# Optimization experiments

Hardware: AMD Instinct MI355X
Metric: run time of the kernel (lower is better)

## Reference

```python
import jax, jax.numpy as jnp
import numpy as np

B, NX, NY = 4, 16384, 16384
CX = CY = 256
CK = CV = 256
H = 8


def setup_inputs() -> dict:
    key = jax.random.key(0)
    ks = jax.random.split(key, 12)
    s = 0.02
    return {
        "x": jax.random.normal(ks[0], (B, NX, CX), jnp.float32),
        "y": jax.random.normal(ks[1], (B, NY, CY), jnp.float32),
        "x_pos_embed": jax.random.normal(ks[2], (B, NX, CX), jnp.float32),
        "y_pos_embed": jax.random.normal(ks[3], (B, NY, CY), jnp.float32),
        "Wq": jax.random.normal(ks[4], (CK, CX), jnp.float32) * s,
        "bq": jnp.zeros((CK,), jnp.float32),
        "Wk": jax.random.normal(ks[5], (CK, CY), jnp.float32) * s,
        "bk": jnp.zeros((CK,), jnp.float32),
        "Wv": jax.random.normal(ks[6], (CV, CY), jnp.float32) * s,
        "bv": jnp.zeros((CV,), jnp.float32),
        "Wr": jax.random.normal(ks[7], (CX, CV), jnp.float32) * s,
        "br": jnp.zeros((CX,), jnp.float32),
    }


def reference(x, y, x_pos_embed, y_pos_embed, Wq, bq, Wk, bk, Wv, bv, Wr, br):
    # Linear projections (nn.Linear: x @ W.T + b)
    q = (x + x_pos_embed) @ Wq.T + bq            # [B, Nx, Ck]
    k = (y + y_pos_embed) @ Wk.T + bk            # [B, Ny, Ck]
    v = y @ Wv.T + bv                            # [B, Ny, Cv]

    dk, dv = CK // H, CV // H
    # Split heads: [B, N, H, d] -> [B, H, N, d]
    q = q.reshape(B, NX, H, dk).transpose(0, 2, 1, 3)
    k = k.reshape(B, NY, H, dk).transpose(0, 2, 1, 3)
    v = v.reshape(B, NY, H, dv).transpose(0, 2, 1, 3)

    # key softmax over tokens (Ny); query softmax over per-head channels (dk)
    k = jax.nn.softmax(k, axis=2)                # [B, H, Ny, dk]
    q = jax.nn.softmax(q, axis=3)                # [B, H, Nx, dk]

    # context = softmax(K)^T V : [B, H, dk, dv]
    context = jnp.einsum('bhnk,bhnv->bhkv', k, v)
    # attended = Q context : [B, H, Nx, dv]
    attended = jnp.einsum('bhnk,bhkv->bhnv', q, context)

    # merge heads -> [B, Nx, Cv], reproject -> [B, Nx, Cx]
    agg = attended.transpose(0, 2, 1, 3).reshape(B, NX, CV)
    return agg @ Wr.T + br
```

## Files before the change

### kernel.cpp

```cpp
#include <hip/hip_runtime.h>


typedef float f32x4 __attribute__((ext_vector_type(4)));
typedef short s16x4 __attribute__((ext_vector_type(4)));
typedef short s16x8 __attribute__((ext_vector_type(8)));

#define MFMA16(A, B, C) __builtin_amdgcn_mfma_f32_16x16x32_bf16((A), (B), (C), 0, 0, 0)

__device__ __forceinline__ short f2bf(float f) {
    unsigned u = __builtin_bit_cast(unsigned, f);
    u = (u + 0x7FFFu + ((u >> 16) & 1u)) >> 16;
    return (short)u;
}
__device__ __forceinline__ float bf2f(short b) {
    unsigned u = ((unsigned)(unsigned short)b) << 16;
    return __builtin_bit_cast(float, u);
}

__global__ __launch_bounds__(256) void wcvt_kernel(
    const float* __restrict__ wq, const float* __restrict__ wk,
    const float* __restrict__ wv, const float* __restrict__ wr,
    short* __restrict__ wbf)
{
    int id = blockIdx.x * 256 + threadIdx.x;
    int m = id >> 13;
    int slot = id & 8191;
    int tile = slot >> 9;
    int ks   = (slot >> 6) & 7;
    int lane = slot & 63;
    int lrow = lane & 15, lgrp = lane >> 4;
    const float* src = (m == 0) ? wq : (m == 1) ? wk : (m == 2) ? wv : wr;
    const float* p = src + (size_t)(tile * 16 + lrow) * 256 + ks * 32 + lgrp * 8;
    f32x4 a = *(const f32x4*)p;
    f32x4 b = *(const f32x4*)(p + 4);
    s16x8 o;
    o[0]=f2bf(a[0]); o[1]=f2bf(a[1]); o[2]=f2bf(a[2]); o[3]=f2bf(a[3]);
    o[4]=f2bf(b[0]); o[5]=f2bf(b[1]); o[6]=f2bf(b[2]); o[7]=f2bf(b[3]);
    *(s16x8*)(wbf + (size_t)id * 8) = o;
}

__global__ __launch_bounds__(256, 4) void kv_kernel(
    const float* __restrict__ y, const float* __restrict__ ypos,
    const short* __restrict__ wkp, const short* __restrict__ wvp,
    const float* __restrict__ bk, const float* __restrict__ bv,
    short* __restrict__ e_buf, short* __restrict__ v_buf)
{
    __shared__ short smem[32 * 512];
    short* ak = smem;
    short* av = smem + 32 * 256;
    const int row0 = blockIdx.x * 32;
    const int t = threadIdx.x;
    const int w = t >> 6, lane = t & 63;

    {
        #pragma unroll
        for (int it = 0; it < 8; ++it) {
            int r = it * 4 + w;
            const float* sy = y    + (size_t)(row0 + r) * 256 + lane * 4;
            const float* sp = ypos + (size_t)(row0 + r) * 256 + lane * 4;
            f32x4 a = *(const f32x4*)sy;
            f32x4 p = *(const f32x4*)sp;
            f32x4 k = a + p;
            s16x4 ov, ok;
            ov[0]=f2bf(a[0]); ov[1]=f2bf(a[1]); ov[2]=f2bf(a[2]); ov[3]=f2bf(a[3]);
            ok[0]=f2bf(k[0]); ok[1]=f2bf(k[1]); ok[2]=f2bf(k[2]); ok[3]=f2bf(k[3]);
            int swz = ((lane >> 1) ^ (r & 7)) * 8 + (lane & 1) * 4;
            *(s16x4*)(av + r * 256 + swz) = ov;
            *(s16x4*)(ak + r * 256 + swz) = ok;
        }
    }
    __syncthreads();

    const int lrow = lane & 15, lgrp = lane >> 4;
    const bool is_k = (w < 2);
    const int colbase = (w & 1) * 128;
    const short* WP = is_k ? wkp : wvp;
    const float* bp = is_k ? bk : bv;
    const short* A = is_k ? ak : av;

    float bias[8];
    #pragma unroll
    for (int nf = 0; nf < 8; ++nf) bias[nf] = bp[colbase + nf * 16 + lrow];

    s16x8 af[2][8];
    #pragma unroll
    for (int mf = 0; mf < 2; ++mf) {
        int rr = mf * 16 + lrow;
        #pragma unroll
        for (int ks = 0; ks < 8; ++ks) {
            int cs = ((ks * 4 + lgrp) ^ (rr & 7));
            af[mf][ks] = *(const s16x8*)(A + rr * 256 + cs * 8);
        }
    }
    __syncthreads();

    #pragma unroll
    for (int nf = 0; nf < 8; ++nf) {
        const int tile = (colbase >> 4) + nf;
        const short* wt = WP + ((size_t)tile * 8) * 512 + lane * 8;
        f32x4 a0 = (f32x4){0.f, 0.f, 0.f, 0.f};
        f32x4 a1 = (f32x4){0.f, 0.f, 0.f, 0.f};
        #pragma unroll
        for (int kg = 0; kg < 2; ++kg) {
            s16x8 bf[4];
            #pragma unroll
            for (int kk = 0; kk < 4; ++kk)
                bf[kk] = *(const s16x8*)(wt + (kg * 4 + kk) * 512);
            #pragma unroll
            for (int kk = 0; kk < 4; ++kk) {
                a0 = MFMA16(af[0][kg * 4 + kk], bf[kk], a0);
                a1 = MFMA16(af[1][kg * 4 + kk], bf[kk], a1);
            }
        }
        const int colp = (is_k ? 0 : 256) + colbase + nf * 16 + lrow;
        #pragma unroll
        for (int rr = 0; rr < 4; ++rr) {
            float v0 = a0[rr] + bias[nf];
            float v1 = a1[rr] + bias[nf];
            if (is_k) { v0 = __expf(v0); v1 = __expf(v1); }
            int lr0 = lgrp * 4 + rr;
            int lr1 = lr0 + 16;
            smem[lr0 * 512 + (((colp >> 3) ^ (lr0 & 7)) * 8) + (colp & 7)] = f2bf(v0);
            smem[lr1 * 512 + (((colp >> 3) ^ (lr1 & 7)) * 8) + (colp & 7)] = f2bf(v1);
        }
    }
    __syncthreads();

    {
        #pragma unroll
        for (int i = 0; i < 8; ++i) {
            int r = i * 4 + w;
            int grow = row0 + r;
            s16x8 val = *(const s16x8*)(smem + r * 512 + (lane ^ (r & 7)) * 8);
            if (lane < 32)
                *(s16x8*)(e_buf + (size_t)grow * 256 + lane * 8) = val;
            else
                *(s16x8*)(v_buf + (size_t)grow * 256 + (lane - 32) * 8) = val;
        }
    }
}

__global__ __launch_bounds__(256) void ctx_kernel(
    const short* __restrict__ e_buf, const short* __restrict__ v_buf,
    float* __restrict__ partials)
{
    __shared__ float se[128 * 32];
    __shared__ float sv[128 * 32];
    __shared__ float red[4 * 1056];
    const int cb = blockIdx.x, bh = blockIdx.y;
    const int b = bh >> 3, h = bh & 7;
    const int tok0 = b * 16384 + cb * 1024;
    const int t = threadIdx.x, w = t >> 6, lane = t & 63;
    const int ckb = (lane >> 3) * 4, cvb = (lane & 7) * 4;

    f32x4 acc[4];
    #pragma unroll
    for (int i = 0; i < 4; ++i) acc[i] = (f32x4){0.f, 0.f, 0.f, 0.f};
    f32x4 dn = (f32x4){0.f, 0.f, 0.f, 0.f};

    for (int it = 0; it < 8; ++it) {
        __syncthreads();
        #pragma unroll
        for (int s = 0; s < 2; ++s) {
            int id = t + s * 256;
            int rr = id >> 2, pp = id & 3;
            size_t g = (size_t)(tok0 + it * 128 + rr) * 256 + h * 32 + pp * 8;
            s16x8 ee = *(const s16x8*)(e_buf + g);
            s16x8 vv = *(const s16x8*)(v_buf + g);
            f32x4 e0 = {bf2f(ee[0]), bf2f(ee[1]), bf2f(ee[2]), bf2f(ee[3])};
            f32x4 e1 = {bf2f(ee[4]), bf2f(ee[5]), bf2f(ee[6]), bf2f(ee[7])};
            f32x4 v0 = {bf2f(vv[0]), bf2f(vv[1]), bf2f(vv[2]), bf2f(vv[3])};
            f32x4 v1 = {bf2f(vv[4]), bf2f(vv[5]), bf2f(vv[6]), bf2f(vv[7])};
            *(f32x4*)(se + rr * 32 + pp * 8)     = e0;
            *(f32x4*)(se + rr * 32 + pp * 8 + 4) = e1;
            *(f32x4*)(sv + rr * 32 + pp * 8)     = v0;
            *(f32x4*)(sv + rr * 32 + pp * 8 + 4) = v1;
        }
        __syncthreads();
        const int r0 = w * 32;
        #pragma unroll 8
        for (int rr = 0; rr < 32; ++rr) {
            f32x4 e4 = *(const f32x4*)(se + (r0 + rr) * 32 + ckb);
            f32x4 v4 = *(const f32x4*)(sv + (r0 + rr) * 32 + cvb);
            acc[0] += e4[0] * v4;
            acc[1] += e4[1] * v4;
            acc[2] += e4[2] * v4;
            acc[3] += e4[3] * v4;
            dn += e4;
        }
    }
    __syncthreads();
    #pragma unroll
    for (int i = 0; i < 4; ++i)
        *(f32x4*)(red + w * 1056 + (ckb + i) * 32 + cvb) = acc[i];
    if ((lane & 7) == 0)
        *(f32x4*)(red + w * 1056 + 1024 + ckb) = dn;
    __syncthreads();
    float* outp = partials + (size_t)(bh * 16 + cb) * 1056;
    for (int e = t; e < 1056; e += 256)
        outp[e] = red[e] + red[1056 + e] + red[2112 + e] + red[3168 + e];
}

__global__ __launch_bounds__(256) void ctx_reduce_kernel(
    const float* __restrict__ partials, short* __restrict__ ctxT)
{
    __shared__ float s[1056];
    const int bh = blockIdx.x, t = threadIdx.x;
    for (int e = t; e < 1056; e += 256) {
        float a = 0.f;
        for (int c = 0; c < 16; ++c) a += partials[(size_t)(bh * 16 + c) * 1056 + e];
        s[e] = a;
    }
    __syncthreads();
    for (int e = t; e < 1024; e += 256) {
        int ck = e >> 5, cv = e & 31;
        float val = s[e] / s[1024 + ck];
        ctxT[(size_t)bh * 1024 + cv * 32 + ck] = f2bf(val);
    }
}

__global__ __launch_bounds__(256, 4) void qout_kernel(
    const float* __restrict__ x, const float* __restrict__ xpos,
    const short* __restrict__ wqp, const float* __restrict__ bq,
    const short* __restrict__ ctxT,
    const short* __restrict__ wrp, const float* __restrict__ br,
    float* __restrict__ out)
{
    __shared__ short alds[32 * 256];
    __shared__ short qlds[4][32 * 64];
    const int row0 = blockIdx.x * 32;
    const int b = row0 >> 14;
    const int t = threadIdx.x;
    const int w = t >> 6, lane = t & 63;

    {
        #pragma unroll
        for (int it = 0; it < 8; ++it) {
            int r = it * 4 + w;
            const float* sx = x    + (size_t)(row0 + r) * 256 + lane * 4;
            const float* sp = xpos + (size_t)(row0 + r) * 256 + lane * 4;
            f32x4 a = *(const f32x4*)sx;
            f32x4 p = *(const f32x4*)sp;
            a += p;
            s16x4 o;
            o[0]=f2bf(a[0]); o[1]=f2bf(a[1]); o[2]=f2bf(a[2]); o[3]=f2bf(a[3]);
            int swz = ((lane >> 1) ^ (r & 7)) * 8 + (lane & 1) * 4;
            *(s16x4*)(alds + r * 256 + swz) = o;
        }
    }
    __syncthreads();

    const int lrow = lane & 15, lgrp = lane >> 4;
    const int wc = w * 64;

    float biasq[4];
    #pragma unroll
    for (int nf = 0; nf < 4; ++nf) biasq[nf] = bq[wc + nf * 16 + lrow];

    f32x4 acc[2][4];
    #pragma unroll
    for (int mf = 0; mf < 2; ++mf)
        #pragma unroll
        for (int nf = 0; nf < 4; ++nf) acc[mf][nf] = (f32x4){0.f, 0.f, 0.f, 0.f};

    #pragma unroll
    for (int ks = 0; ks < 8; ++ks) {
        s16x8 af[2];
        #pragma unroll
        for (int mf = 0; mf < 2; ++mf) {
            int rr = mf * 16 + lrow;
            int cs = (ks * 4 + lgrp) ^ (rr & 7);
            af[mf] = *(const s16x8*)(alds + rr * 256 + cs * 8);
        }
        #pragma unroll
        for (int nf = 0; nf < 4; ++nf) {
            int tile = (wc >> 4) + nf;
            s16x8 bfr = *(const s16x8*)(wqp + ((size_t)tile * 8 + ks) * 512 + lane * 8);
            acc[0][nf] = MFMA16(af[0], bfr, acc[0][nf]);
            acc[1][nf] = MFMA16(af[1], bfr, acc[1][nf]);
        }
    }

    short* ql = (short*)qlds[w];
    #pragma unroll
    for (int mf = 0; mf < 2; ++mf) {
        f32x4 e[4];
        #pragma unroll
        for (int nf = 0; nf < 4; ++nf)
            #pragma unroll
            for (int rr = 0; rr < 4; ++rr)
                e[nf][rr] = __expf(acc[mf][nf][rr] + biasq[nf]);
        #pragma unroll
        for (int hl = 0; hl < 2; ++hl) {
            #pragma unroll
            for (int rr = 0; rr < 4; ++rr) {
                float s = e[hl * 2][rr] + e[hl * 2 + 1][rr];
                s += __shfl_xor(s, 1);
                s += __shfl_xor(s, 2);
                s += __shfl_xor(s, 4);
                s += __shfl_xor(s, 8);
                float rinv = 1.0f / s;
                int row = mf * 16 + lgrp * 4 + rr;
                #pragma unroll
                for (int n2 = 0; n2 < 2; ++n2) {
                    int colc = hl * 32 + n2 * 16 + lrow;
                    int cs = (colc >> 3) ^ (row & 7);
                    ql[row * 64 + cs * 8 + (colc & 7)] = f2bf(e[hl * 2 + n2][rr] * rinv);
                }
            }
        }
    }
    __syncthreads();

    f32x4 att[2][2][2];
    #pragma unroll
    for (int hl = 0; hl < 2; ++hl)
        #pragma unroll
        for (int mf = 0; mf < 2; ++mf)
            #pragma unroll
            for (int n2 = 0; n2 < 2; ++n2) att[hl][mf][n2] = (f32x4){0.f,0.f,0.f,0.f};

    #pragma unroll
    for (int hl = 0; hl < 2; ++hl) {
        const short* cbase = ctxT + (size_t)(b * 8 + w * 2 + hl) * 1024;
        s16x8 bctx[2];
        #pragma unroll
        for (int n2 = 0; n2 < 2; ++n2)
            bctx[n2] = *(const s16x8*)(cbase + (n2 * 16 + lrow) * 32 + lgrp * 8);
        #pragma unroll
        for (int mf = 0; mf < 2; ++mf) {
            int row = mf * 16 + lrow;
            int cs = (hl * 4 + lgrp) ^ (row & 7);
            s16x8 aq = *(const s16x8*)(ql + row * 64 + cs * 8);
            #pragma unroll
            for (int n2 = 0; n2 < 2; ++n2)
                att[hl][mf][n2] = MFMA16(aq, bctx[n2], att[hl][mf][n2]);
        }
    }

    #pragma unroll
    for (int hl = 0; hl < 2; ++hl)
      #pragma unroll
      for (int mf = 0; mf < 2; ++mf)
        #pragma unroll
        for (int n2 = 0; n2 < 2; ++n2)
          #pragma unroll
          for (int rr = 0; rr < 4; ++rr) {
              int row = mf * 16 + lgrp * 4 + rr;
              int col = wc + hl * 32 + n2 * 16 + lrow;
              int cs = (col >> 3) ^ (row & 7);
              alds[row * 256 + cs * 8 + (col & 7)] = f2bf(att[hl][mf][n2][rr]);
          }
    __syncthreads();

    float biasr[4];
    #pragma unroll
    for (int nf = 0; nf < 4; ++nf) biasr[nf] = br[wc + nf * 16 + lrow];

    f32x4 acc2[2][4];
    #pragma unroll
    for (int mf = 0; mf < 2; ++mf)
        #pragma unroll
        for (int nf = 0; nf < 4; ++nf) acc2[mf][nf] = (f32x4){0.f, 0.f, 0.f, 0.f};

    #pragma unroll
    for (int ks = 0; ks < 8; ++ks) {
        s16x8 af[2];
        #pragma unroll
        for (int mf = 0; mf < 2; ++mf) {
            int rr = mf * 16 + lrow;
            int cs = (ks * 4 + lgrp) ^ (rr & 7);
            af[mf] = *(const s16x8*)(alds + rr * 256 + cs * 8);
        }
        #pragma unroll
        for (int nf = 0; nf < 4; ++nf) {
            int tile = (wc >> 4) + nf;
            s16x8 bfr = *(const s16x8*)(wrp + ((size_t)tile * 8 + ks) * 512 + lane * 8);
            acc2[0][nf] = MFMA16(af[0], bfr, acc2[0][nf]);
            acc2[1][nf] = MFMA16(af[1], bfr, acc2[1][nf]);
        }
    }

    #pragma unroll
    for (int mf = 0; mf < 2; ++mf)
      #pragma unroll
      for (int nf = 0; nf < 4; ++nf)
        #pragma unroll
        for (int rr = 0; rr < 4; ++rr) {
            int grow = row0 + mf * 16 + lgrp * 4 + rr;
            out[(size_t)grow * 256 + wc + nf * 16 + lrow] = acc2[mf][nf][rr] + biasr[nf];
        }
}

extern "C" void kernel_launch(void* const* d_in, const int* in_sizes, int n_in,
                              void* d_out, int out_size, void* d_ws, size_t ws_size,
                              hipStream_t stream)
{
    const float* x    = (const float*)d_in[0];
    const float* y    = (const float*)d_in[1];
    const float* xpos = (const float*)d_in[2];
    const float* ypos = (const float*)d_in[3];
    const float* Wq   = (const float*)d_in[4];
    const float* bq   = (const float*)d_in[5];
    const float* Wk   = (const float*)d_in[6];
    const float* bk   = (const float*)d_in[7];
    const float* Wv   = (const float*)d_in[8];
    const float* bv   = (const float*)d_in[9];
    const float* Wr   = (const float*)d_in[10];
    const float* br   = (const float*)d_in[11];

    char*  ws    = (char*)d_ws;
    short* wbf   = (short*)(ws);
    short* ctxT  = (short*)(ws + 524288);
    float* parts = (float*)(ws + (1 << 20));
    short* e_buf = (short*)(ws + ((size_t)4 << 20));
    short* v_buf = e_buf + (size_t)65536 * 256;
    float* outp  = (float*)d_out;

    hipLaunchKernelGGL(wcvt_kernel, dim3(128), dim3(256), 0, stream,
                       Wq, Wk, Wv, Wr, wbf);
    hipLaunchKernelGGL(kv_kernel, dim3(2048), dim3(256), 0, stream,
                       y, ypos, wbf + 65536, wbf + 131072, bk, bv, e_buf, v_buf);
    hipLaunchKernelGGL(ctx_kernel, dim3(16, 32), dim3(256), 0, stream,
                       e_buf, v_buf, parts);
    hipLaunchKernelGGL(ctx_reduce_kernel, dim3(32), dim3(256), 0, stream,
                       parts, ctxT);
    hipLaunchKernelGGL(qout_kernel, dim3(2048), dim3(256), 0, stream,
                       x, xpos, wbf, bq, ctxT, wbf + 196608, br, outp);
}
```

Baseline: 169.1 us.

## Use 512-thread blocks in kv and qout kernels, one 16-row tile per wave

```diff
diff --git a/kernel.cpp b/kernel.cpp
--- a/kernel.cpp
+++ b/kernel.cpp
@@ -39,7 +39,7 @@
     *(s16x8*)(wbf + (size_t)id * 8) = o;
 }
 
-__global__ __launch_bounds__(256, 4) void kv_kernel(
+__global__ __launch_bounds__(512, 6) void kv_kernel(
     const float* __restrict__ y, const float* __restrict__ ypos,
     const short* __restrict__ wkp, const short* __restrict__ wvp,
     const float* __restrict__ bk, const float* __restrict__ bv,
@@ -54,12 +54,10 @@
 
     {
         #pragma unroll
-        for (int it = 0; it < 8; ++it) {
-            int r = it * 4 + w;
-            const float* sy = y    + (size_t)(row0 + r) * 256 + lane * 4;
-            const float* sp = ypos + (size_t)(row0 + r) * 256 + lane * 4;
-            f32x4 a = *(const f32x4*)sy;
-            f32x4 p = *(const f32x4*)sp;
+        for (int it = 0; it < 4; ++it) {
+            int r = it * 8 + w;
+            f32x4 a = *(const f32x4*)(y    + (size_t)(row0 + r) * 256 + lane * 4);
+            f32x4 p = *(const f32x4*)(ypos + (size_t)(row0 + r) * 256 + lane * 4);
             f32x4 k = a + p;
             s16x4 ov, ok;
             ov[0]=f2bf(a[0]); ov[1]=f2bf(a[1]); ov[2]=f2bf(a[2]); ov[3]=f2bf(a[3]);
@@ -72,8 +70,12 @@
     __syncthreads();
 
     const int lrow = lane & 15, lgrp = lane >> 4;
-    const bool is_k = (w < 2);
-    const int colbase = (w & 1) * 128;
+    const bool is_k = (w < 4);
+    const int sub = w & 3;
+    const int rh = sub >> 1;
+    const int ch = sub & 1;
+    const int colbase = ch * 128;
+    const int tile0 = ch * 8;
     const short* WP = is_k ? wkp : wvp;
     const float* bp = is_k ? bk : bv;
     const short* A = is_k ? ak : av;
@@ -82,56 +84,46 @@
     #pragma unroll
     for (int nf = 0; nf < 8; ++nf) bias[nf] = bp[colbase + nf * 16 + lrow];
 
-    s16x8 af[2][8];
-    #pragma unroll
-    for (int mf = 0; mf < 2; ++mf) {
-        int rr = mf * 16 + lrow;
+    s16x8 af[8];
+    {
+        int rr = rh * 16 + lrow;
         #pragma unroll
         for (int ks = 0; ks < 8; ++ks) {
             int cs = ((ks * 4 + lgrp) ^ (rr & 7));
-            af[mf][ks] = *(const s16x8*)(A + rr * 256 + cs * 8);
+            af[ks] = *(const s16x8*)(A + rr * 256 + cs * 8);
         }
     }
     __syncthreads();
 
     #pragma unroll
     for (int nf = 0; nf < 8; ++nf) {
-        const int tile = (colbase >> 4) + nf;
+        const int tile = tile0 + nf;
         const short* wt = WP + ((size_t)tile * 8) * 512 + lane * 8;
         f32x4 a0 = (f32x4){0.f, 0.f, 0.f, 0.f};
-        f32x4 a1 = (f32x4){0.f, 0.f, 0.f, 0.f};
-        #pragma unroll
-        for (int kg = 0; kg < 2; ++kg) {
-            s16x8 bf[4];
-            #pragma unroll
-            for (int kk = 0; kk < 4; ++kk)
-                bf[kk] = *(const s16x8*)(wt + (kg * 4 + kk) * 512);
-            #pragma unroll
-            for (int kk = 0; kk < 4; ++kk) {
-                a0 = MFMA16(af[0][kg * 4 + kk], bf[kk], a0);
-                a1 = MFMA16(af[1][kg * 4 + kk], bf[kk], a1);
-            }
+        #pragma unroll
+        for (int kg = 0; kg < 4; ++kg) {
+            s16x8 b0 = *(const s16x8*)(wt + (kg * 2 + 0) * 512);
+            s16x8 b1 = *(const s16x8*)(wt + (kg * 2 + 1) * 512);
+            a0 = MFMA16(af[kg * 2 + 0], b0, a0);
+            a0 = MFMA16(af[kg * 2 + 1], b1, a0);
         }
         const int colp = (is_k ? 0 : 256) + colbase + nf * 16 + lrow;
         #pragma unroll
         for (int rr = 0; rr < 4; ++rr) {
             float v0 = a0[rr] + bias[nf];
-            float v1 = a1[rr] + bias[nf];
-            if (is_k) { v0 = __expf(v0); v1 = __expf(v1); }
-            int lr0 = lgrp * 4 + rr;
-            int lr1 = lr0 + 16;
-            smem[lr0 * 512 + (((colp >> 3) ^ (lr0 & 7)) * 8) + (colp & 7)] = f2bf(v0);
-            smem[lr1 * 512 + (((colp >> 3) ^ (lr1 & 7)) * 8) + (colp & 7)] = f2bf(v1);
-        }
-    }
-    __syncthreads();
-
-    {
-        #pragma unroll
-        for (int i = 0; i < 8; ++i) {
-            int r = i * 4 + w;
+            if (is_k) v0 = __expf(v0);
+            int lr = rh * 16 + lgrp * 4 + rr;
+            smem[lr * 512 + (((colp >> 3) ^ (lr & 7)) * 8) + (colp & 7)] = f2bf(v0);
+        }
+    }
+    __syncthreads();
+
+    {
+        #pragma unroll
+        for (int i = 0; i < 4; ++i) {
+            int r = i * 8 + w;
             int grow = row0 + r;
-            s16x8 val = *(const s16x8*)(smem + r * 512 + (lane ^ (r & 7)) * 8);
+            s16x8 val = *(const s16x8*)(smem + r * 512 + ((lane ^ (r & 7)) << 3));
             if (lane < 32)
                 *(s16x8*)(e_buf + (size_t)grow * 256 + lane * 8) = val;
             else
@@ -219,7 +211,7 @@
     }
 }
 
-__global__ __launch_bounds__(256, 4) void qout_kernel(
+__global__ __launch_bounds__(512, 6) void qout_kernel(
     const float* __restrict__ x, const float* __restrict__ xpos,
     const short* __restrict__ wqp, const float* __restrict__ bq,
     const short* __restrict__ ctxT,
@@ -227,7 +219,7 @@
     float* __restrict__ out)
 {
     __shared__ short alds[32 * 256];
-    __shared__ short qlds[4][32 * 64];
+    __shared__ short qlds[8][16 * 64];
     const int row0 = blockIdx.x * 32;
     const int b = row0 >> 14;
     const int t = threadIdx.x;
@@ -235,12 +227,10 @@
 
     {
         #pragma unroll
-        for (int it = 0; it < 8; ++it) {
-            int r = it * 4 + w;
-            const float* sx = x    + (size_t)(row0 + r) * 256 + lane * 4;
-            const float* sp = xpos + (size_t)(row0 + r) * 256 + lane * 4;
-            f32x4 a = *(const f32x4*)sx;
-            f32x4 p = *(const f32x4*)sp;
+        for (int it = 0; it < 4; ++it) {
+            int r = it * 8 + w;
+            f32x4 a = *(const f32x4*)(x    + (size_t)(row0 + r) * 256 + lane * 4);
+            f32x4 p = *(const f32x4*)(xpos + (size_t)(row0 + r) * 256 + lane * 4);
             a += p;
             s16x4 o;
             o[0]=f2bf(a[0]); o[1]=f2bf(a[1]); o[2]=f2bf(a[2]); o[3]=f2bf(a[3]);
@@ -251,45 +241,49 @@
     __syncthreads();
 
     const int lrow = lane & 15, lgrp = lane >> 4;
-    const int wc = w * 64;
+    const int rh = w >> 2;
+    const int q4 = w & 3;
+    const int wc = q4 * 64;
+    const int tile0 = wc >> 4;
 
     float biasq[4];
     #pragma unroll
     for (int nf = 0; nf < 4; ++nf) biasq[nf] = bq[wc + nf * 16 + lrow];
 
-    f32x4 acc[2][4];
-    #pragma unroll
-    for (int mf = 0; mf < 2; ++mf)
-        #pragma unroll
-        for (int nf = 0; nf < 4; ++nf) acc[mf][nf] = (f32x4){0.f, 0.f, 0.f, 0.f};
-
-    #pragma unroll
-    for (int ks = 0; ks < 8; ++ks) {
-        s16x8 af[2];
-        #pragma unroll
-        for (int mf = 0; mf < 2; ++mf) {
-            int rr = mf * 16 + lrow;
+    s16x8 af[8];
+    {
+        int rr = rh * 16 + lrow;
+        #pragma unroll
+        for (int ks = 0; ks < 8; ++ks) {
             int cs = (ks * 4 + lgrp) ^ (rr & 7);
-            af[mf] = *(const s16x8*)(alds + rr * 256 + cs * 8);
-        }
-        #pragma unroll
-        for (int nf = 0; nf < 4; ++nf) {
-            int tile = (wc >> 4) + nf;
-            s16x8 bfr = *(const s16x8*)(wqp + ((size_t)tile * 8 + ks) * 512 + lane * 8);
-            acc[0][nf] = MFMA16(af[0], bfr, acc[0][nf]);
-            acc[1][nf] = MFMA16(af[1], bfr, acc[1][nf]);
+            af[ks] = *(const s16x8*)(alds + rr * 256 + cs * 8);
+        }
+    }
+
+    f32x4 acc[4];
+    #pragma unroll
+    for (int nf = 0; nf < 4; ++nf) acc[nf] = (f32x4){0.f, 0.f, 0.f, 0.f};
+
+    #pragma unroll
+    for (int nf = 0; nf < 4; ++nf) {
+        const short* wt = wqp + ((size_t)(tile0 + nf) * 8) * 512 + lane * 8;
+        #pragma unroll
+        for (int kg = 0; kg < 4; ++kg) {
+            s16x8 b0 = *(const s16x8*)(wt + (kg * 2 + 0) * 512);
+            s16x8 b1 = *(const s16x8*)(wt + (kg * 2 + 1) * 512);
+            acc[nf] = MFMA16(af[kg * 2 + 0], b0, acc[nf]);
+            acc[nf] = MFMA16(af[kg * 2 + 1], b1, acc[nf]);
         }
     }
 
     short* ql = (short*)qlds[w];
-    #pragma unroll
-    for (int mf = 0; mf < 2; ++mf) {
+    {
         f32x4 e[4];
         #pragma unroll
         for (int nf = 0; nf < 4; ++nf)
             #pragma unroll
             for (int rr = 0; rr < 4; ++rr)
-                e[nf][rr] = __expf(acc[mf][nf][rr] + biasq[nf]);
+                e[nf][rr] = __expf(acc[nf][rr] + biasq[nf]);
         #pragma unroll
         for (int hl = 0; hl < 2; ++hl) {
             #pragma unroll
@@ -300,95 +294,84 @@
                 s += __shfl_xor(s, 4);
                 s += __shfl_xor(s, 8);
                 float rinv = 1.0f / s;
-                int row = mf * 16 + lgrp * 4 + rr;
+                int lr = lgrp * 4 + rr;
                 #pragma unroll
                 for (int n2 = 0; n2 < 2; ++n2) {
                     int colc = hl * 32 + n2 * 16 + lrow;
-                    int cs = (colc >> 3) ^ (row & 7);
-                    ql[row * 64 + cs * 8 + (colc & 7)] = f2bf(e[hl * 2 + n2][rr] * rinv);
+                    int cs = (colc >> 3) ^ (lr & 7);
+                    ql[lr * 64 + cs * 8 + (colc & 7)] = f2bf(e[hl * 2 + n2][rr] * rinv);
                 }
             }
         }
     }
     __syncthreads();
 
-    f32x4 att[2][2][2];
+    f32x4 att[2][2];
     #pragma unroll
     for (int hl = 0; hl < 2; ++hl)
         #pragma unroll
-        for (int mf = 0; mf < 2; ++mf)
-            #pragma unroll
-            for (int n2 = 0; n2 < 2; ++n2) att[hl][mf][n2] = (f32x4){0.f,0.f,0.f,0.f};
+        for (int n2 = 0; n2 < 2; ++n2) att[hl][n2] = (f32x4){0.f,0.f,0.f,0.f};
 
     #pragma unroll
     for (int hl = 0; hl < 2; ++hl) {
-        const short* cbase = ctxT + (size_t)(b * 8 + w * 2 + hl) * 1024;
-        s16x8 bctx[2];
-        #pragma unroll
-        for (int n2 = 0; n2 < 2; ++n2)
-            bctx[n2] = *(const s16x8*)(cbase + (n2 * 16 + lrow) * 32 + lgrp * 8);
-        #pragma unroll
-        for (int mf = 0; mf < 2; ++mf) {
-            int row = mf * 16 + lrow;
-            int cs = (hl * 4 + lgrp) ^ (row & 7);
-            s16x8 aq = *(const s16x8*)(ql + row * 64 + cs * 8);
-            #pragma unroll
-            for (int n2 = 0; n2 < 2; ++n2)
-                att[hl][mf][n2] = MFMA16(aq, bctx[n2], att[hl][mf][n2]);
-        }
+        const short* cbase = ctxT + (size_t)(b * 8 + q4 * 2 + hl) * 1024;
+        s16x8 bctx0 = *(const s16x8*)(cbase + (0 * 16 + lrow) * 32 + lgrp * 8);
+        s16x8 bctx1 = *(const s16x8*)(cbase + (1 * 16 + lrow) * 32 + lgrp * 8);
+        int cs = (hl * 4 + lgrp) ^ (lrow & 7);
+        s16x8 aq = *(const s16x8*)(ql + lrow * 64 + cs * 8);
+        att[hl][0] = MFMA16(aq, bctx0, att[hl][0]);
+        att[hl][1] = MFMA16(aq, bctx1, att[hl][1]);
     }
 
     #pragma unroll
     for (int hl = 0; hl < 2; ++hl)
       #pragma unroll
-      for (int mf = 0; mf < 2; ++mf)
-        #pragma unroll
-        for (int n2 = 0; n2 < 2; ++n2)
-          #pragma unroll
-          for (int rr = 0; rr < 4; ++rr) {
-              int row = mf * 16 + lgrp * 4 + rr;
-              int col = wc + hl * 32 + n2 * 16 + lrow;
-              int cs = (col >> 3) ^ (row & 7);
-              alds[row * 256 + cs * 8 + (col & 7)] = f2bf(att[hl][mf][n2][rr]);
-          }
+      for (int n2 = 0; n2 < 2; ++n2)
+        #pragma unroll
+        for (int rr = 0; rr < 4; ++rr) {
+            int row = rh * 16 + lgrp * 4 + rr;
+            int col = wc + hl * 32 + n2 * 16 + lrow;
+            int cs = (col >> 3) ^ (row & 7);
+            alds[row * 256 + cs * 8 + (col & 7)] = f2bf(att[hl][n2][rr]);
+        }
     __syncthreads();
 
     float biasr[4];
     #pragma unroll
     for (int nf = 0; nf < 4; ++nf) biasr[nf] = br[wc + nf * 16 + lrow];
 
-    f32x4 acc2[2][4];
-    #pragma unroll
-    for (int mf = 0; mf < 2; ++mf)
-        #pragma unroll
-        for (int nf = 0; nf < 4; ++nf) acc2[mf][nf] = (f32x4){0.f, 0.f, 0.f, 0.f};
-
-    #pragma unroll
-    for (int ks = 0; ks < 8; ++ks) {
-        s16x8 af[2];
-        #pragma unroll
-        for (int mf = 0; mf < 2; ++mf) {
-            int rr = mf * 16 + lrow;
+    s16x8 af2[8];
+    {
+        int rr = rh * 16 + lrow;
+        #pragma unroll
+        for (int ks = 0; ks < 8; ++ks) {
             int cs = (ks * 4 + lgrp) ^ (rr & 7);
-            af[mf] = *(const s16x8*)(alds + rr * 256 + cs * 8);
-        }
-        #pragma unroll
-        for (int nf = 0; nf < 4; ++nf) {
-            int tile = (wc >> 4) + nf;
-            s16x8 bfr = *(const s16x8*)(wrp + ((size_t)tile * 8 + ks) * 512 + lane * 8);
-            acc2[0][nf] = MFMA16(af[0], bfr, acc2[0][nf]);
-            acc2[1][nf] = MFMA16(af[1], bfr, acc2[1][nf]);
-        }
-    }
-
-    #pragma unroll
-    for (int mf = 0; mf < 2; ++mf)
-      #pragma unroll
-      for (int nf = 0; nf < 4; ++nf)
+            af2[ks] = *(const s16x8*)(alds + rr * 256 + cs * 8);
+        }
+    }
+
+    f32x4 acc2[4];
+    #pragma unroll
+    for (int nf = 0; nf < 4; ++nf) acc2[nf] = (f32x4){0.f, 0.f, 0.f, 0.f};
+
+    #pragma unroll
+    for (int nf = 0; nf < 4; ++nf) {
+        const short* wt = wrp + ((size_t)(tile0 + nf) * 8) * 512 + lane * 8;
+        #pragma unroll
+        for (int kg = 0; kg < 4; ++kg) {
+            s16x8 b0 = *(const s16x8*)(wt + (kg * 2 + 0) * 512);
+            s16x8 b1 = *(const s16x8*)(wt + (kg * 2 + 1) * 512);
+            acc2[nf] = MFMA16(af2[kg * 2 + 0], b0, acc2[nf]);
+            acc2[nf] = MFMA16(af2[kg * 2 + 1], b1, acc2[nf]);
+        }
+    }
+
+    #pragma unroll
+    for (int nf = 0; nf < 4; ++nf)
         #pragma unroll
         for (int rr = 0; rr < 4; ++rr) {
-            int grow = row0 + mf * 16 + lgrp * 4 + rr;
-            out[(size_t)grow * 256 + wc + nf * 16 + lrow] = acc2[mf][nf][rr] + biasr[nf];
+            int grow = row0 + rh * 16 + lgrp * 4 + rr;
+            out[(size_t)grow * 256 + wc + nf * 16 + lrow] = acc2[nf][rr] + biasr[nf];
         }
 }
 
@@ -419,12 +402,12 @@
 
     hipLaunchKernelGGL(wcvt_kernel, dim3(128), dim3(256), 0, stream,
                        Wq, Wk, Wv, Wr, wbf);
-    hipLaunchKernelGGL(kv_kernel, dim3(2048), dim3(256), 0, stream,
+    hipLaunchKernelGGL(kv_kernel, dim3(2048), dim3(512), 0, stream,
                        y, ypos, wbf + 65536, wbf + 131072, bk, bv, e_buf, v_buf);
     hipLaunchKernelGGL(ctx_kernel, dim3(16, 32), dim3(256), 0, stream,
                        e_buf, v_buf, parts);
     hipLaunchKernelGGL(ctx_reduce_kernel, dim3(32), dim3(256), 0, stream,
                        parts, ctxT);
-    hipLaunchKernelGGL(qout_kernel, dim3(2048), dim3(256), 0, stream,
+    hipLaunchKernelGGL(qout_kernel, dim3(2048), dim3(512), 0, stream,
                        x, xpos, wbf, bq, ctxT, wbf + 196608, br, outp);
 }
```

Result: slower. 187.8 us (+11.1%).
